# Kernel optimization log

Measured on AMD Instinct MI355X. Metric: run time of the kernel, lower is better.

The kernel has to match this reference:

```python
import jax, jax.numpy as jnp
import numpy as np

B, S, D, H, E, K = 4, 2048, 1024, 2048, 8, 2


def setup_inputs() -> dict:
    key = jax.random.key(0)
    ks = jax.random.split(key, 5)
    x = jax.random.normal(ks[0], (B, S, D), dtype=jnp.float32)
    Wr = jax.random.normal(ks[1], (D, E), dtype=jnp.float32) * 0.02  # router weight
    w1 = jax.random.normal(ks[2], (E, D, H), dtype=jnp.float32) * 0.02  # gate proj per expert
    w3 = jax.random.normal(ks[3], (E, D, H), dtype=jnp.float32) * 0.02  # up proj per expert
    w2 = jax.random.normal(ks[4], (E, H, D), dtype=jnp.float32) * 0.02  # down proj per expert
    return {"x": x, "Wr": Wr, "w1": w1, "w2": w2, "w3": w3}


def reference(x, Wr, w1, w2, w3):
    b, s, d = x.shape
    e = Wr.shape[1]
    flat = x.reshape(b * s, d)                      # [T, D]
    logits = flat @ Wr                              # [T, E]
    probs = jax.nn.softmax(logits, axis=-1)
    vals, idx = jax.lax.top_k(probs, K)             # [T, K]
    weights = vals / jnp.sum(vals, axis=-1, keepdims=True)
    onehot = jax.nn.one_hot(idx, e, dtype=flat.dtype)   # [T, K, E]
    cw = jnp.einsum('tke,tk->te', onehot, weights)      # combine weight per (token, expert)

    # naive dense: every expert computes every token, masked by combine weights
    out = jnp.zeros_like(flat)
    for ei in range(e):  # fixed small structural loop over experts
        h = jax.nn.silu(flat @ w1[ei]) * (flat @ w3[ei])   # [T, H]
        out = out + (h @ w2[ei]) * cw[:, ei:ei + 1]

    # aux load-balancing loss (usage uses any() over top-k slots, as in torch code)
    usage = (onehot.sum(axis=1) > 0).astype(flat.dtype).mean(axis=0)  # [E]
    prob_mass = probs.mean(axis=0)                                     # [E]
    aux_loss = e * jnp.sum(usage * prob_mass)
    return out.reshape(b, s, d), aux_loss
```

## Files before the change

kernel.cpp:

```cpp
#include <hip/hip_runtime.h>
#include <hip/hip_bf16.h>
#include <cstdint>
#include <cstddef>

#define T_TOK 8192
#define DIM   1024
#define HID   2048
#define NE    8
#define CAP   2816

#define SLOT  32768

typedef __attribute__((ext_vector_type(8))) short bf16x8;
typedef __attribute__((ext_vector_type(4))) float f32x4;
using bf16 = __hip_bfloat16;

__device__ __forceinline__ void gload16(const bf16* g, bf16* l) {
    __builtin_amdgcn_global_load_lds(
        (const __attribute__((address_space(1))) unsigned int*)(g),
        (__attribute__((address_space(3))) unsigned int*)(l), 16, 0, 0);
}
__device__ __forceinline__ float b2f(unsigned short u) {
    return __uint_as_float(((unsigned int)u) << 16);
}
#define MFMA16(a, b, c) __builtin_amdgcn_mfma_f32_16x16x32_bf16((a), (b), (c), 0, 0, 0)
#define BARRIER() asm volatile("s_barrier" ::: "memory")
#define WAITVM8() asm volatile("s_waitcnt vmcnt(8)" ::: "memory")
#define WAITVM0() asm volatile("s_waitcnt vmcnt(0)" ::: "memory")

__global__ __launch_bounds__(256) void k_transpose_all(const float* __restrict__ w1,
                                                       const float* __restrict__ w3,
                                                       const float* __restrict__ w2,
                                                       bf16* __restrict__ w1t,
                                                       bf16* __restrict__ w3t,
                                                       bf16* __restrict__ w2t) {
    __shared__ float tile[64][65];
    int z = blockIdx.z;
    const float* in = (z == 0) ? w1 : (z == 1) ? w3 : w2;
    bf16* out = (z == 0) ? w1t : (z == 1) ? w3t : w2t;
    int R = (z == 2) ? HID : DIM;
    int C = (z == 2) ? DIM : HID;
    int e = blockIdx.y;
    int ct = C >> 6;
    int r0 = (blockIdx.x / ct) << 6;
    int c0 = (blockIdx.x % ct) << 6;
    const float* src = in + (size_t)e * R * C;
    bf16* dst = out + (size_t)e * R * C;
    int s = threadIdx.x & 15, g = threadIdx.x >> 4;
#pragma unroll
    for (int j = 0; j < 4; ++j) {
        int row = j * 16 + g;
        float4 v = *(const float4*)(src + (size_t)(r0 + row) * C + c0 + s * 4);
        tile[row][s * 4 + 0] = v.x; tile[row][s * 4 + 1] = v.y;
        tile[row][s * 4 + 2] = v.z; tile[row][s * 4 + 3] = v.w;
    }
    __syncthreads();
#pragma unroll
    for (int j = 0; j < 4; ++j) {
        int c = j * 16 + g;
        int r = s * 4;
        bf16 o[4] = {__float2bfloat16(tile[r][c]),     __float2bfloat16(tile[r + 1][c]),
                     __float2bfloat16(tile[r + 2][c]), __float2bfloat16(tile[r + 3][c])};
        *(uint2*)(dst + (size_t)(c0 + c) * R + r0 + r) = *(const uint2*)o;
    }
}

__global__ __launch_bounds__(256) void k_logits(const float* __restrict__ x,
                                                const float* __restrict__ Wr,
                                                float* __restrict__ logits,
                                                bf16* __restrict__ xb) {
    __shared__ float wl[NE][DIM];
    for (int o = threadIdx.x; o < NE * DIM; o += 256) {
        int e = o >> 10, d = o & (DIM - 1);
        wl[e][d] = Wr[d * NE + e];
    }
    __syncthreads();
    int wid = threadIdx.x >> 6, lane = threadIdx.x & 63;
    int t = blockIdx.x * 4 + wid;
    const float* xr = x + (size_t)t * DIM;
    double acc[NE];
#pragma unroll
    for (int e = 0; e < NE; ++e) acc[e] = 0.0;
#pragma unroll
    for (int i = 0; i < DIM / 256; ++i) {
        int base = i * 256 + lane * 4;
        float4 v = *(const float4*)(xr + base);
        bf16 o[4] = {__float2bfloat16(v.x), __float2bfloat16(v.y),
                     __float2bfloat16(v.z), __float2bfloat16(v.w)};
        *(uint2*)(xb + (size_t)t * DIM + base) = *(const uint2*)o;
#pragma unroll
        for (int e = 0; e < NE; ++e)
            acc[e] += (double)v.x * wl[e][base] + (double)v.y * wl[e][base + 1]
                    + (double)v.z * wl[e][base + 2] + (double)v.w * wl[e][base + 3];
    }
#pragma unroll
    for (int e = 0; e < NE; ++e) {
        double v = acc[e];
        for (int m = 32; m >= 1; m >>= 1) v += __shfl_xor(v, m);
        if (lane == 0) logits[t * NE + e] = (float)v;
    }
}

__global__ __launch_bounds__(256) void k_route(const float* __restrict__ logits,
                                               int* counts, int* seg_tok, float* seg_w,
                                               int* slotpos, float* probsum) {
    int t = blockIdx.x * 256 + threadIdx.x;
    float l[NE];
#pragma unroll
    for (int e = 0; e < NE; ++e) l[e] = logits[t * NE + e];
    float mx = l[0];
#pragma unroll
    for (int e = 1; e < NE; ++e) mx = fmaxf(mx, l[e]);
    float p[NE], s = 0.f;
#pragma unroll
    for (int e = 0; e < NE; ++e) { p[e] = expf(l[e] - mx); s += p[e]; }
    float inv = 1.f / s;
#pragma unroll
    for (int e = 0; e < NE; ++e) p[e] *= inv;
    int e0 = 0; float v0 = p[0];
#pragma unroll
    for (int e = 1; e < NE; ++e) if (p[e] > v0) { v0 = p[e]; e0 = e; }
    int e1 = -1; float v1 = -1.f;
#pragma unroll
    for (int e = 0; e < NE; ++e) if (e != e0 && p[e] > v1) { v1 = p[e]; e1 = e; }
    float wsum = v0 + v1;
    float w0 = v0 / wsum, w1 = v1 / wsum;

    int lane = threadIdx.x & 63, wid = threadIdx.x >> 6;
    __shared__ float ps[4][NE];
#pragma unroll
    for (int e = 0; e < NE; ++e) {
        float v = p[e];
        for (int m = 32; m >= 1; m >>= 1) v += __shfl_xor(v, m);
        if (lane == 0) ps[wid][e] = v;
    }
    __syncthreads();
    if (threadIdx.x < NE) {
        float v = ps[0][threadIdx.x] + ps[1][threadIdx.x] + ps[2][threadIdx.x] + ps[3][threadIdx.x];
        atomicAdd(&probsum[threadIdx.x], v);
    }
    for (int slot = 0; slot < 2; ++slot) {
        int   e  = slot ? e1 : e0;
        float wv = slot ? w1 : w0;
#pragma unroll
        for (int ex = 0; ex < NE; ++ex) {
            unsigned long long m = __ballot(e == ex);
            if (e == ex) {
                int leader = __ffsll(m) - 1;
                int base = 0;
                if (lane == leader) base = atomicAdd(&counts[ex], __popcll(m));
                base = __shfl(base, leader);
                int pos = base + (int)__popcll(m & ((1ull << lane) - 1ull));
                if (pos < CAP) {
                    seg_tok[ex * CAP + pos] = t;
                    seg_w[ex * CAP + pos]  = wv;
                    slotpos[2 * t + slot]  = ex * CAP + pos;
                } else {
                    slotpos[2 * t + slot]  = -1;
                }
            }
        }
    }
}

__global__ __launch_bounds__(512, 2) void k_gemm1(const bf16* __restrict__ xb,
                                                  const bf16* __restrict__ w1t,
                                                  const bf16* __restrict__ w3t,
                                                  const int* __restrict__ counts,
                                                  const int* __restrict__ seg_tok,
                                                  bf16* __restrict__ h) {
    __shared__ __align__(16) bf16 lds[2 * SLOT];
    __shared__ int toks[256];
    const int NTL = HID / 128;
    int flat = blockIdx.y * gridDim.x + blockIdx.x;
    int cpx  = (gridDim.x * NE) >> 3;
    int swz  = (flat & 7) * cpx + (flat >> 3);
    int e    = swz / gridDim.x;
    int tile = swz % gridDim.x;
    int mtile = tile / NTL, ntile = tile % NTL;
    int cnt = counts[e]; if (cnt > CAP) cnt = CAP;
    if (mtile * 256 >= cnt) return;

    int tx = threadIdx.x, lane = tx & 63, wid = tx >> 6;
    for (int i = tx; i < 256; i += 512) {
        int slot = mtile * 256 + i;
        toks[i] = seg_tok[e * CAP + (slot < cnt ? slot : 0)];
    }
    __syncthreads();

    int l3 = lane >> 3, l7 = lane & 7, l15 = lane & 15, lh = lane >> 4;
    int swzco = (l7 ^ l3) << 3;
    const bf16* ap0 = xb + (size_t)toks[  0 + wid * 8 + l3] * DIM + swzco;
    const bf16* ap1 = xb + (size_t)toks[ 64 + wid * 8 + l3] * DIM + swzco;
    const bf16* ap2 = xb + (size_t)toks[128 + wid * 8 + l3] * DIM + swzco;
    const bf16* ap3 = xb + (size_t)toks[192 + wid * 8 + l3] * DIM + swzco;
    const bf16* bg0 = w1t + ((size_t)e * HID + ntile * 128 +  0 + wid * 8 + l3) * DIM + swzco;
    const bf16* bg1 = w1t + ((size_t)e * HID + ntile * 128 + 64 + wid * 8 + l3) * DIM + swzco;
    const bf16* bu0 = w3t + ((size_t)e * HID + ntile * 128 +  0 + wid * 8 + l3) * DIM + swzco;
    const bf16* bu1 = w3t + ((size_t)e * HID + ntile * 128 + 64 + wid * 8 + l3) * DIM + swzco;
    int wbase = wid * 512;
    int wm = wid >> 2, wn = wid & 3;

    f32x4 accg[8][2], accu[8][2];
    f32x4 zero4 = {0.f, 0.f, 0.f, 0.f};
#pragma unroll
    for (int m = 0; m < 8; ++m)
#pragma unroll
        for (int n = 0; n < 2; ++n) { accg[m][n] = zero4; accu[m][n] = zero4; }

#define G1_STAGE(ss, ko) do { \
        gload16(ap0 + (ko), lds + (ss) +     0 + wbase); \
        gload16(ap1 + (ko), lds + (ss) +  4096 + wbase); \
        gload16(ap2 + (ko), lds + (ss) +  8192 + wbase); \
        gload16(ap3 + (ko), lds + (ss) + 12288 + wbase); \
        gload16(bg0 + (ko), lds + (ss) + 16384 + wbase); \
        gload16(bg1 + (ko), lds + (ss) + 20480 + wbase); \
        gload16(bu0 + (ko), lds + (ss) + 24576 + wbase); \
        gload16(bu1 + (ko), lds + (ss) + 28672 + wbase); } while (0)

#define G1_PHASE(cs, mh, ks) do { \
        int cex = ((((ks) << 2) | lh) ^ l7) << 3; \
        const bf16* Ab = lds + (cs) + (wm * 128 + (mh) * 64 + l15) * 64 + cex; \
        bf16x8 a0 = *(const bf16x8*)(Ab); \
        bf16x8 a1 = *(const bf16x8*)(Ab + 1024); \
        bf16x8 a2 = *(const bf16x8*)(Ab + 2048); \
        bf16x8 a3 = *(const bf16x8*)(Ab + 3072); \
        const bf16* Bb = lds + (cs) + 16384 + (wn * 32 + l15) * 64 + cex; \
        bf16x8 g0 = *(const bf16x8*)(Bb); \
        bf16x8 g1 = *(const bf16x8*)(Bb + 1024); \
        bf16x8 u0 = *(const bf16x8*)(Bb + 8192); \
        bf16x8 u1 = *(const bf16x8*)(Bb + 9216); \
        __builtin_amdgcn_s_setprio(1); \
        accg[(mh)*4+0][0] = MFMA16(a0, g0, accg[(mh)*4+0][0]); \
        accg[(mh)*4+1][0] = MFMA16(a1, g0, accg[(mh)*4+1][0]); \
        accg[(mh)*4+2][0] = MFMA16(a2, g0, accg[(mh)*4+2][0]); \
        accg[(mh)*4+3][0] = MFMA16(a3, g0, accg[(mh)*4+3][0]); \
        accg[(mh)*4+0][1] = MFMA16(a0, g1, accg[(mh)*4+0][1]); \
        accg[(mh)*4+1][1] = MFMA16(a1, g1, accg[(mh)*4+1][1]); \
        accg[(mh)*4+2][1] = MFMA16(a2, g1, accg[(mh)*4+2][1]); \
        accg[(mh)*4+3][1] = MFMA16(a3, g1, accg[(mh)*4+3][1]); \
        accu[(mh)*4+0][0] = MFMA16(a0, u0, accu[(mh)*4+0][0]); \
        accu[(mh)*4+1][0] = MFMA16(a1, u0, accu[(mh)*4+1][0]); \
        accu[(mh)*4+2][0] = MFMA16(a2, u0, accu[(mh)*4+2][0]); \
        accu[(mh)*4+3][0] = MFMA16(a3, u0, accu[(mh)*4+3][0]); \
        accu[(mh)*4+0][1] = MFMA16(a0, u1, accu[(mh)*4+0][1]); \
        accu[(mh)*4+1][1] = MFMA16(a1, u1, accu[(mh)*4+1][1]); \
        accu[(mh)*4+2][1] = MFMA16(a2, u1, accu[(mh)*4+2][1]); \
        accu[(mh)*4+3][1] = MFMA16(a3, u1, accu[(mh)*4+3][1]); \
        __builtin_amdgcn_s_setprio(0); } while (0)

    G1_STAGE(0, 0);
    const int NT = DIM / 64;
    int cs = 0, ns = SLOT;
#pragma unroll 1
    for (int T = 0; T < NT; ++T) {
        if (T + 1 < NT) { G1_STAGE(ns, (T + 1) * 64); WAITVM8(); }
        else WAITVM0();
        BARRIER();
        G1_PHASE(cs, 0, 0); G1_PHASE(cs, 0, 1);
        G1_PHASE(cs, 1, 0); G1_PHASE(cs, 1, 1);
        BARRIER();
        int tmp = cs; cs = ns; ns = tmp;
    }

    bf16* hdst = h + ((size_t)e * CAP + (size_t)mtile * 256) * HID + ntile * 128;
#pragma unroll
    for (int m = 0; m < 8; ++m)
#pragma unroll
        for (int n = 0; n < 2; ++n)
#pragma unroll
            for (int r = 0; r < 4; ++r) {
                int row = wm * 128 + m * 16 + lh * 4 + r;
                int col = wn * 32 + n * 16 + l15;
                float gg = accg[m][n][r], uu = accu[m][n][r];
                float hv = gg / (1.f + __expf(-gg)) * uu;
                hdst[(size_t)row * HID + col] = __float2bfloat16(hv);
            }
#undef G1_STAGE
#undef G1_PHASE
}

__global__ __launch_bounds__(512, 2) void k_gemm2(const bf16* __restrict__ h,
                                                  const bf16* __restrict__ w2t,
                                                  const int* __restrict__ counts,
                                                  const float* __restrict__ seg_w,
                                                  bf16* __restrict__ ybuf) {
    __shared__ __align__(16) bf16 lds[2 * SLOT];
    __shared__ float wts[256];
    const int NTL = DIM / 256;
    int flat = blockIdx.y * gridDim.x + blockIdx.x;
    int cpx  = (gridDim.x * NE) >> 3;
    int swz  = (flat & 7) * cpx + (flat >> 3);
    int e    = swz / gridDim.x;
    int tile = swz % gridDim.x;
    int mtile = tile / NTL, ntile = tile % NTL;
    int cnt = counts[e]; if (cnt > CAP) cnt = CAP;
    if (mtile * 256 >= cnt) return;

    int tx = threadIdx.x, lane = tx & 63, wid = tx >> 6;
    for (int i = tx; i < 256; i += 512) {
        int slot = mtile * 256 + i;
        wts[i] = (slot < cnt) ? seg_w[e * CAP + slot] : 0.f;
    }
    __syncthreads();

    int l3 = lane >> 3, l7 = lane & 7, l15 = lane & 15, lh = lane >> 4;
    int swzco = (l7 ^ l3) << 3;
    const bf16* ap0 = h + ((size_t)e * CAP + mtile * 256 +   0 + wid * 8 + l3) * HID + swzco;
    const bf16* ap1 = h + ((size_t)e * CAP + mtile * 256 +  64 + wid * 8 + l3) * HID + swzco;
    const bf16* ap2 = h + ((size_t)e * CAP + mtile * 256 + 128 + wid * 8 + l3) * HID + swzco;
    const bf16* ap3 = h + ((size_t)e * CAP + mtile * 256 + 192 + wid * 8 + l3) * HID + swzco;
    const bf16* bp0 = w2t + ((size_t)e * DIM + ntile * 256 +   0 + wid * 8 + l3) * HID + swzco;
    const bf16* bp1 = w2t + ((size_t)e * DIM + ntile * 256 +  64 + wid * 8 + l3) * HID + swzco;
    const bf16* bp2 = w2t + ((size_t)e * DIM + ntile * 256 + 128 + wid * 8 + l3) * HID + swzco;
    const bf16* bp3 = w2t + ((size_t)e * DIM + ntile * 256 + 192 + wid * 8 + l3) * HID + swzco;
    int wbase = wid * 512;
    int wm = wid >> 2, wn = wid & 3;

    f32x4 acc[8][4];
    f32x4 zero4 = {0.f, 0.f, 0.f, 0.f};
#pragma unroll
    for (int m = 0; m < 8; ++m)
#pragma unroll
        for (int n = 0; n < 4; ++n) acc[m][n] = zero4;

#define G2_STAGE(ss, ko) do { \
        gload16(ap0 + (ko), lds + (ss) +     0 + wbase); \
        gload16(ap1 + (ko), lds + (ss) +  4096 + wbase); \
        gload16(ap2 + (ko), lds + (ss) +  8192 + wbase); \
        gload16(ap3 + (ko), lds + (ss) + 12288 + wbase); \
        gload16(bp0 + (ko), lds + (ss) + 16384 + wbase); \
        gload16(bp1 + (ko), lds + (ss) + 20480 + wbase); \
        gload16(bp2 + (ko), lds + (ss) + 24576 + wbase); \
        gload16(bp3 + (ko), lds + (ss) + 28672 + wbase); } while (0)

#define G2_PHASE(cs, mh, ks) do { \
        int cex = ((((ks) << 2) | lh) ^ l7) << 3; \
        const bf16* Ab = lds + (cs) + (wm * 128 + (mh) * 64 + l15) * 64 + cex; \
        bf16x8 a0 = *(const bf16x8*)(Ab); \
        bf16x8 a1 = *(const bf16x8*)(Ab + 1024); \
        bf16x8 a2 = *(const bf16x8*)(Ab + 2048); \
        bf16x8 a3 = *(const bf16x8*)(Ab + 3072); \
        const bf16* Bb = lds + (cs) + 16384 + (wn * 64 + l15) * 64 + cex; \
        bf16x8 b0 = *(const bf16x8*)(Bb); \
        bf16x8 b1 = *(const bf16x8*)(Bb + 1024); \
        bf16x8 b2 = *(const bf16x8*)(Bb + 2048); \
        bf16x8 b3 = *(const bf16x8*)(Bb + 3072); \
        __builtin_amdgcn_s_setprio(1); \
        acc[(mh)*4+0][0] = MFMA16(a0, b0, acc[(mh)*4+0][0]); \
        acc[(mh)*4+1][0] = MFMA16(a1, b0, acc[(mh)*4+1][0]); \
        acc[(mh)*4+2][0] = MFMA16(a2, b0, acc[(mh)*4+2][0]); \
        acc[(mh)*4+3][0] = MFMA16(a3, b0, acc[(mh)*4+3][0]); \
        acc[(mh)*4+0][1] = MFMA16(a0, b1, acc[(mh)*4+0][1]); \
        acc[(mh)*4+1][1] = MFMA16(a1, b1, acc[(mh)*4+1][1]); \
        acc[(mh)*4+2][1] = MFMA16(a2, b1, acc[(mh)*4+2][1]); \
        acc[(mh)*4+3][1] = MFMA16(a3, b1, acc[(mh)*4+3][1]); \
        acc[(mh)*4+0][2] = MFMA16(a0, b2, acc[(mh)*4+0][2]); \
        acc[(mh)*4+1][2] = MFMA16(a1, b2, acc[(mh)*4+1][2]); \
        acc[(mh)*4+2][2] = MFMA16(a2, b2, acc[(mh)*4+2][2]); \
        acc[(mh)*4+3][2] = MFMA16(a3, b2, acc[(mh)*4+3][2]); \
        acc[(mh)*4+0][3] = MFMA16(a0, b3, acc[(mh)*4+0][3]); \
        acc[(mh)*4+1][3] = MFMA16(a1, b3, acc[(mh)*4+1][3]); \
        acc[(mh)*4+2][3] = MFMA16(a2, b3, acc[(mh)*4+2][3]); \
        acc[(mh)*4+3][3] = MFMA16(a3, b3, acc[(mh)*4+3][3]); \
        __builtin_amdgcn_s_setprio(0); } while (0)

    G2_STAGE(0, 0);
    const int NT = HID / 64;
    int cs = 0, ns = SLOT;
#pragma unroll 1
    for (int T = 0; T < NT; ++T) {
        if (T + 1 < NT) { G2_STAGE(ns, (T + 1) * 64); WAITVM8(); }
        else WAITVM0();
        BARRIER();
        G2_PHASE(cs, 0, 0); G2_PHASE(cs, 0, 1);
        G2_PHASE(cs, 1, 0); G2_PHASE(cs, 1, 1);
        BARRIER();
        int tmp = cs; cs = ns; ns = tmp;
    }

    bf16* ydst = ybuf + ((size_t)e * CAP + (size_t)mtile * 256) * DIM + ntile * 256;
#pragma unroll
    for (int m = 0; m < 8; ++m)
#pragma unroll
        for (int n = 0; n < 4; ++n)
#pragma unroll
            for (int r = 0; r < 4; ++r) {
                int row = wm * 128 + m * 16 + lh * 4 + r;
                int col = wn * 64 + n * 16 + l15;
                ydst[(size_t)row * DIM + col] = __float2bfloat16(acc[m][n][r] * wts[row]);
            }
#undef G2_STAGE
#undef G2_PHASE
}

__global__ __launch_bounds__(256) void k_combine(const bf16* __restrict__ yb,
                                                 const int* __restrict__ slotpos,
                                                 float* __restrict__ out) {
    int t = blockIdx.x;
    int s0 = slotpos[2 * t], s1 = slotpos[2 * t + 1];
    int d = threadIdx.x * 4;
    float4 a = {0.f, 0.f, 0.f, 0.f};
    if (s0 >= 0) {
        ushort4 v = *(const ushort4*)(yb + (size_t)s0 * DIM + d);
        a.x += b2f(v.x); a.y += b2f(v.y); a.z += b2f(v.z); a.w += b2f(v.w);
    }
    if (s1 >= 0) {
        ushort4 v = *(const ushort4*)(yb + (size_t)s1 * DIM + d);
        a.x += b2f(v.x); a.y += b2f(v.y); a.z += b2f(v.z); a.w += b2f(v.w);
    }
    *(float4*)(out + (size_t)t * DIM + d) = a;
}

__global__ void k_aux(const int* __restrict__ counts, const float* __restrict__ probsum,
                      float* __restrict__ outaux) {
    if (threadIdx.x == 0 && blockIdx.x == 0) {
        float s = 0.f;
        for (int e = 0; e < NE; ++e)
            s += ((float)counts[e] / (float)T_TOK) * (probsum[e] / (float)T_TOK);
        *outaux = (float)NE * s;
    }
}

extern "C" void kernel_launch(void* const* d_in, const int* in_sizes, int n_in,
                              void* d_out, int out_size, void* d_ws, size_t ws_size,
                              hipStream_t stream) {
    const float* x  = (const float*)d_in[0];
    const float* Wr = (const float*)d_in[1];
    const float* w1 = (const float*)d_in[2];
    const float* w2 = (const float*)d_in[3];
    const float* w3 = (const float*)d_in[4];
    float* out = (float*)d_out;

    char* ws = (char*)d_ws;
    size_t off = 0;
    auto alloc = [&](size_t bytes) { void* p = ws + off; off += (bytes + 255) & ~(size_t)255; return p; };
    bf16*  xb      = (bf16*)alloc((size_t)T_TOK * DIM * 2);
    bf16*  w1t     = (bf16*)alloc((size_t)NE * HID * DIM * 2);
    bf16*  w3t     = (bf16*)alloc((size_t)NE * HID * DIM * 2);
    bf16*  w2t     = (bf16*)alloc((size_t)NE * DIM * HID * 2);
    bf16*  hbuf    = (bf16*)alloc((size_t)NE * CAP * HID * 2);
    float* logits  = (float*)alloc((size_t)T_TOK * NE * 4);
    int*   counts  = (int*)alloc(256);
    int*   segtok  = (int*)alloc((size_t)NE * CAP * 4);
    float* segw    = (float*)alloc((size_t)NE * CAP * 4);
    int*   slotpos = (int*)alloc((size_t)T_TOK * 2 * 4);
    float* probsum = (float*)alloc(256);
    bf16*  ybuf    = w1t;
    (void)ws_size; (void)in_sizes; (void)n_in;

    hipMemsetAsync(counts, 0, 256, stream);
    hipMemsetAsync(probsum, 0, 256, stream);

    k_logits<<<T_TOK / 4, 256, 0, stream>>>(x, Wr, logits, xb);
    k_route<<<T_TOK / 256, 256, 0, stream>>>(logits, counts, segtok, segw, slotpos, probsum);

    dim3 gt((DIM / 64) * (HID / 64), NE, 3);
    k_transpose_all<<<gt, 256, 0, stream>>>(w1, w3, w2, w1t, w3t, w2t);

    dim3 g1((CAP / 256) * (HID / 128), NE);
    k_gemm1<<<g1, 512, 0, stream>>>(xb, w1t, w3t, counts, segtok, hbuf);
    dim3 g2((CAP / 256) * (DIM / 256), NE);
    k_gemm2<<<g2, 512, 0, stream>>>(hbuf, w2t, counts, segw, ybuf);

    k_combine<<<T_TOK, 256, 0, stream>>>(ybuf, slotpos, out);
    k_aux<<<1, 64, 0, stream>>>(counts, probsum, out + (size_t)T_TOK * DIM);
}
```

Measured before the change: 459.4 us.

## Switch GEMM mainloops to 4-stage BK=32 pipeline with split A/B staging

Both expert GEMM kernels move from a double-buffered K=64 tile to a four-slot ring of K=32 tiles with prefetch distance two. A and B loads are issued separately: A for step k+2 before the first barrier, B after the first half of the MFMAs. The LDS layout and XOR swizzle change to match 32-wide rows. The aim is to hide global-load latency better and keep loads in flight across barriers. The cost is two barriers per smaller K step, a more intricate vmcnt wait schedule, and a risk of bank conflicts with the new swizzle.

New measurement: 471.9 us. 2.7% more time.

```diff
diff --git a/kernel.cpp b/kernel.cpp
--- a/kernel.cpp
+++ b/kernel.cpp
@@ -9,8 +9,6 @@
 #define NE    8
 #define CAP   2816
 
-#define SLOT  32768
-
 typedef __attribute__((ext_vector_type(8))) short bf16x8;
 typedef __attribute__((ext_vector_type(4))) float f32x4;
 using bf16 = __hip_bfloat16;
@@ -25,7 +23,8 @@
 }
 #define MFMA16(a, b, c) __builtin_amdgcn_mfma_f32_16x16x32_bf16((a), (b), (c), 0, 0, 0)
 #define BARRIER() asm volatile("s_barrier" ::: "memory")
-#define WAITVM8() asm volatile("s_waitcnt vmcnt(8)" ::: "memory")
+#define WAITVM6() asm volatile("s_waitcnt vmcnt(6)" ::: "memory")
+#define WAITVM4() asm volatile("s_waitcnt vmcnt(4)" ::: "memory")
 #define WAITVM0() asm volatile("s_waitcnt vmcnt(0)" ::: "memory")
 
 __global__ __launch_bounds__(256) void k_transpose_all(const float* __restrict__ w1,
@@ -169,7 +168,7 @@
                                                   const int* __restrict__ counts,
                                                   const int* __restrict__ seg_tok,
                                                   bf16* __restrict__ h) {
-    __shared__ __align__(16) bf16 lds[2 * SLOT];
+    __shared__ __align__(16) bf16 lds[65536];
     __shared__ int toks[256];
     const int NTL = HID / 128;
     int flat = blockIdx.y * gridDim.x + blockIdx.x;
@@ -188,18 +187,20 @@
     }
     __syncthreads();
 
-    int l3 = lane >> 3, l7 = lane & 7, l15 = lane & 15, lh = lane >> 4;
-    int swzco = (l7 ^ l3) << 3;
-    const bf16* ap0 = xb + (size_t)toks[  0 + wid * 8 + l3] * DIM + swzco;
-    const bf16* ap1 = xb + (size_t)toks[ 64 + wid * 8 + l3] * DIM + swzco;
-    const bf16* ap2 = xb + (size_t)toks[128 + wid * 8 + l3] * DIM + swzco;
-    const bf16* ap3 = xb + (size_t)toks[192 + wid * 8 + l3] * DIM + swzco;
-    const bf16* bg0 = w1t + ((size_t)e * HID + ntile * 128 +  0 + wid * 8 + l3) * DIM + swzco;
-    const bf16* bg1 = w1t + ((size_t)e * HID + ntile * 128 + 64 + wid * 8 + l3) * DIM + swzco;
-    const bf16* bu0 = w3t + ((size_t)e * HID + ntile * 128 +  0 + wid * 8 + l3) * DIM + swzco;
-    const bf16* bu1 = w3t + ((size_t)e * HID + ntile * 128 + 64 + wid * 8 + l3) * DIM + swzco;
-    int wbase = wid * 512;
+    int sr  = tx >> 2;
+    int sc8 = (((tx & 3) ^ ((tx >> 3) & 3)) << 3);
+    const bf16* sApLo = xb + (size_t)toks[sr]       * DIM + sc8;
+    const bf16* sApHi = xb + (size_t)toks[128 + sr] * DIM + sc8;
+    const bf16* sBg   = w1t + ((size_t)e * HID + ntile * 128 + sr) * DIM + sc8;
+    const bf16* sBu   = w3t + ((size_t)e * HID + ntile * 128 + sr) * DIM + sc8;
+    bf16* dA = lds + tx * 8;
+    bf16* dB = lds + 32768 + tx * 8;
+
+    int l15 = lane & 15, lh = lane >> 4;
     int wm = wid >> 2, wn = wid & 3;
+    int ach = ((lh ^ ((l15 >> 1) & 3)) << 3);
+    const bf16* rA = lds + (wm * 128 + l15) * 32 + ach;
+    const bf16* rB = lds + 32768 + (wn * 32 + l15) * 32 + ach;
 
     f32x4 accg[8][2], accu[8][2];
     f32x4 zero4 = {0.f, 0.f, 0.f, 0.f};
@@ -208,60 +209,70 @@
 #pragma unroll
         for (int n = 0; n < 2; ++n) { accg[m][n] = zero4; accu[m][n] = zero4; }
 
-#define G1_STAGE(ss, ko) do { \
-        gload16(ap0 + (ko), lds + (ss) +     0 + wbase); \
-        gload16(ap1 + (ko), lds + (ss) +  4096 + wbase); \
-        gload16(ap2 + (ko), lds + (ss) +  8192 + wbase); \
-        gload16(ap3 + (ko), lds + (ss) + 12288 + wbase); \
-        gload16(bg0 + (ko), lds + (ss) + 16384 + wbase); \
-        gload16(bg1 + (ko), lds + (ss) + 20480 + wbase); \
-        gload16(bu0 + (ko), lds + (ss) + 24576 + wbase); \
-        gload16(bu1 + (ko), lds + (ss) + 28672 + wbase); } while (0)
-
-#define G1_PHASE(cs, mh, ks) do { \
-        int cex = ((((ks) << 2) | lh) ^ l7) << 3; \
-        const bf16* Ab = lds + (cs) + (wm * 128 + (mh) * 64 + l15) * 64 + cex; \
-        bf16x8 a0 = *(const bf16x8*)(Ab); \
-        bf16x8 a1 = *(const bf16x8*)(Ab + 1024); \
-        bf16x8 a2 = *(const bf16x8*)(Ab + 2048); \
-        bf16x8 a3 = *(const bf16x8*)(Ab + 3072); \
-        const bf16* Bb = lds + (cs) + 16384 + (wn * 32 + l15) * 64 + cex; \
-        bf16x8 g0 = *(const bf16x8*)(Bb); \
-        bf16x8 g1 = *(const bf16x8*)(Bb + 1024); \
-        bf16x8 u0 = *(const bf16x8*)(Bb + 8192); \
-        bf16x8 u1 = *(const bf16x8*)(Bb + 9216); \
-        __builtin_amdgcn_s_setprio(1); \
-        accg[(mh)*4+0][0] = MFMA16(a0, g0, accg[(mh)*4+0][0]); \
-        accg[(mh)*4+1][0] = MFMA16(a1, g0, accg[(mh)*4+1][0]); \
-        accg[(mh)*4+2][0] = MFMA16(a2, g0, accg[(mh)*4+2][0]); \
-        accg[(mh)*4+3][0] = MFMA16(a3, g0, accg[(mh)*4+3][0]); \
-        accg[(mh)*4+0][1] = MFMA16(a0, g1, accg[(mh)*4+0][1]); \
-        accg[(mh)*4+1][1] = MFMA16(a1, g1, accg[(mh)*4+1][1]); \
-        accg[(mh)*4+2][1] = MFMA16(a2, g1, accg[(mh)*4+2][1]); \
-        accg[(mh)*4+3][1] = MFMA16(a3, g1, accg[(mh)*4+3][1]); \
-        accu[(mh)*4+0][0] = MFMA16(a0, u0, accu[(mh)*4+0][0]); \
-        accu[(mh)*4+1][0] = MFMA16(a1, u0, accu[(mh)*4+1][0]); \
-        accu[(mh)*4+2][0] = MFMA16(a2, u0, accu[(mh)*4+2][0]); \
-        accu[(mh)*4+3][0] = MFMA16(a3, u0, accu[(mh)*4+3][0]); \
-        accu[(mh)*4+0][1] = MFMA16(a0, u1, accu[(mh)*4+0][1]); \
-        accu[(mh)*4+1][1] = MFMA16(a1, u1, accu[(mh)*4+1][1]); \
-        accu[(mh)*4+2][1] = MFMA16(a2, u1, accu[(mh)*4+2][1]); \
-        accu[(mh)*4+3][1] = MFMA16(a3, u1, accu[(mh)*4+3][1]); \
-        __builtin_amdgcn_s_setprio(0); } while (0)
-
-    G1_STAGE(0, 0);
-    const int NT = DIM / 64;
-    int cs = 0, ns = SLOT;
+#define STAGE_A1(s, ko) do { \
+        gload16(sApLo + (ko), dA + (s) * 8192); \
+        gload16(sApHi + (ko), dA + (s) * 8192 + 4096); } while (0)
+#define STAGE_B1(s, ko) do { \
+        gload16(sBg + (ko), dB + (s) * 8192); \
+        gload16(sBu + (ko), dB + (s) * 8192 + 4096); } while (0)
+
+    STAGE_A1(0, 0);  STAGE_B1(0, 0);
+    STAGE_A1(1, 32); STAGE_B1(1, 32);
+
+    const int NT = DIM / 32;
+    bf16x8 g0, g1, u0, u1;
 #pragma unroll 1
-    for (int T = 0; T < NT; ++T) {
-        if (T + 1 < NT) { G1_STAGE(ns, (T + 1) * 64); WAITVM8(); }
-        else WAITVM0();
+    for (int k = 0; k < NT; ++k) {
+        int cs = (k & 3) * 8192, ps = (k + 2) & 3;
+        bool st = (k + 2 < NT);
+        int ko = (k + 2) * 32;
+        if (st) STAGE_A1(ps, ko);
+        if (k < NT - 2) WAITVM6(); else if (k < NT - 1) WAITVM4(); else WAITVM0();
         BARRIER();
-        G1_PHASE(cs, 0, 0); G1_PHASE(cs, 0, 1);
-        G1_PHASE(cs, 1, 0); G1_PHASE(cs, 1, 1);
+        {
+            const bf16* Ab = rA + cs;
+            bf16x8 a0 = *(const bf16x8*)(Ab);
+            bf16x8 a1 = *(const bf16x8*)(Ab + 512);
+            bf16x8 a2 = *(const bf16x8*)(Ab + 1024);
+            bf16x8 a3 = *(const bf16x8*)(Ab + 1536);
+            const bf16* Bb = rB + cs;
+            g0 = *(const bf16x8*)(Bb);
+            g1 = *(const bf16x8*)(Bb + 512);
+            u0 = *(const bf16x8*)(Bb + 4096);
+            u1 = *(const bf16x8*)(Bb + 4608);
+            __builtin_amdgcn_s_setprio(1);
+            accg[0][0] = MFMA16(a0, g0, accg[0][0]); accg[1][0] = MFMA16(a1, g0, accg[1][0]);
+            accg[2][0] = MFMA16(a2, g0, accg[2][0]); accg[3][0] = MFMA16(a3, g0, accg[3][0]);
+            accg[0][1] = MFMA16(a0, g1, accg[0][1]); accg[1][1] = MFMA16(a1, g1, accg[1][1]);
+            accg[2][1] = MFMA16(a2, g1, accg[2][1]); accg[3][1] = MFMA16(a3, g1, accg[3][1]);
+            accu[0][0] = MFMA16(a0, u0, accu[0][0]); accu[1][0] = MFMA16(a1, u0, accu[1][0]);
+            accu[2][0] = MFMA16(a2, u0, accu[2][0]); accu[3][0] = MFMA16(a3, u0, accu[3][0]);
+            accu[0][1] = MFMA16(a0, u1, accu[0][1]); accu[1][1] = MFMA16(a1, u1, accu[1][1]);
+            accu[2][1] = MFMA16(a2, u1, accu[2][1]); accu[3][1] = MFMA16(a3, u1, accu[3][1]);
+            __builtin_amdgcn_s_setprio(0);
+        }
+        if (st) STAGE_B1(ps, ko);
         BARRIER();
-        int tmp = cs; cs = ns; ns = tmp;
-    }
+        {
+            const bf16* Ab = rA + cs + 2048;
+            bf16x8 a4 = *(const bf16x8*)(Ab);
+            bf16x8 a5 = *(const bf16x8*)(Ab + 512);
+            bf16x8 a6 = *(const bf16x8*)(Ab + 1024);
+            bf16x8 a7 = *(const bf16x8*)(Ab + 1536);
+            __builtin_amdgcn_s_setprio(1);
+            accg[4][0] = MFMA16(a4, g0, accg[4][0]); accg[5][0] = MFMA16(a5, g0, accg[5][0]);
+            accg[6][0] = MFMA16(a6, g0, accg[6][0]); accg[7][0] = MFMA16(a7, g0, accg[7][0]);
+            accg[4][1] = MFMA16(a4, g1, accg[4][1]); accg[5][1] = MFMA16(a5, g1, accg[5][1]);
+            accg[6][1] = MFMA16(a6, g1, accg[6][1]); accg[7][1] = MFMA16(a7, g1, accg[7][1]);
+            accu[4][0] = MFMA16(a4, u0, accu[4][0]); accu[5][0] = MFMA16(a5, u0, accu[5][0]);
+            accu[6][0] = MFMA16(a6, u0, accu[6][0]); accu[7][0] = MFMA16(a7, u0, accu[7][0]);
+            accu[4][1] = MFMA16(a4, u1, accu[4][1]); accu[5][1] = MFMA16(a5, u1, accu[5][1]);
+            accu[6][1] = MFMA16(a6, u1, accu[6][1]); accu[7][1] = MFMA16(a7, u1, accu[7][1]);
+            __builtin_amdgcn_s_setprio(0);
+        }
+    }
+#undef STAGE_A1
+#undef STAGE_B1
 
     bf16* hdst = h + ((size_t)e * CAP + (size_t)mtile * 256) * HID + ntile * 128;
 #pragma unroll
@@ -276,8 +287,6 @@
                 float hv = gg / (1.f + __expf(-gg)) * uu;
                 hdst[(size_t)row * HID + col] = __float2bfloat16(hv);
             }
-#undef G1_STAGE
-#undef G1_PHASE
 }
 
 __global__ __launch_bounds__(512, 2) void k_gemm2(const bf16* __restrict__ h,
@@ -285,7 +294,7 @@
                                                   const int* __restrict__ counts,
                                                   const float* __restrict__ seg_w,
                                                   bf16* __restrict__ ybuf) {
-    __shared__ __align__(16) bf16 lds[2 * SLOT];
+    __shared__ __align__(16) bf16 lds[65536];
     __shared__ float wts[256];
     const int NTL = DIM / 256;
     int flat = blockIdx.y * gridDim.x + blockIdx.x;
@@ -304,18 +313,20 @@
     }
     __syncthreads();
 
-    int l3 = lane >> 3, l7 = lane & 7, l15 = lane & 15, lh = lane >> 4;
-    int swzco = (l7 ^ l3) << 3;
-    const bf16* ap0 = h + ((size_t)e * CAP + mtile * 256 +   0 + wid * 8 + l3) * HID + swzco;
-    const bf16* ap1 = h + ((size_t)e * CAP + mtile * 256 +  64 + wid * 8 + l3) * HID + swzco;
-    const bf16* ap2 = h + ((size_t)e * CAP + mtile * 256 + 128 + wid * 8 + l3) * HID + swzco;
-    const bf16* ap3 = h + ((size_t)e * CAP + mtile * 256 + 192 + wid * 8 + l3) * HID + swzco;
-    const bf16* bp0 = w2t + ((size_t)e * DIM + ntile * 256 +   0 + wid * 8 + l3) * HID + swzco;
-    const bf16* bp1 = w2t + ((size_t)e * DIM + ntile * 256 +  64 + wid * 8 + l3) * HID + swzco;
-    const bf16* bp2 = w2t + ((size_t)e * DIM + ntile * 256 + 128 + wid * 8 + l3) * HID + swzco;
-    const bf16* bp3 = w2t + ((size_t)e * DIM + ntile * 256 + 192 + wid * 8 + l3) * HID + swzco;
-    int wbase = wid * 512;
+    int sr  = tx >> 2;
+    int sc8 = (((tx & 3) ^ ((tx >> 3) & 3)) << 3);
+    const bf16* sApLo = h + ((size_t)e * CAP + mtile * 256 + sr) * HID + sc8;
+    const bf16* sApHi = h + ((size_t)e * CAP + mtile * 256 + 128 + sr) * HID + sc8;
+    const bf16* sBpLo = w2t + ((size_t)e * DIM + ntile * 256 + sr) * HID + sc8;
+    const bf16* sBpHi = w2t + ((size_t)e * DIM + ntile * 256 + 128 + sr) * HID + sc8;
+    bf16* dA = lds + tx * 8;
+    bf16* dB = lds + 32768 + tx * 8;
+
+    int l15 = lane & 15, lh = lane >> 4;
     int wm = wid >> 2, wn = wid & 3;
+    int ach = ((lh ^ ((l15 >> 1) & 3)) << 3);
+    const bf16* rA = lds + (wm * 128 + l15) * 32 + ach;
+    const bf16* rB = lds + 32768 + (wn * 64 + l15) * 32 + ach;
 
     f32x4 acc[8][4];
     f32x4 zero4 = {0.f, 0.f, 0.f, 0.f};
@@ -324,60 +335,70 @@
 #pragma unroll
         for (int n = 0; n < 4; ++n) acc[m][n] = zero4;
 
-#define G2_STAGE(ss, ko) do { \
-        gload16(ap0 + (ko), lds + (ss) +     0 + wbase); \
-        gload16(ap1 + (ko), lds + (ss) +  4096 + wbase); \
-        gload16(ap2 + (ko), lds + (ss) +  8192 + wbase); \
-        gload16(ap3 + (ko), lds + (ss) + 12288 + wbase); \
-        gload16(bp0 + (ko), lds + (ss) + 16384 + wbase); \
-        gload16(bp1 + (ko), lds + (ss) + 20480 + wbase); \
-        gload16(bp2 + (ko), lds + (ss) + 24576 + wbase); \
-        gload16(bp3 + (ko), lds + (ss) + 28672 + wbase); } while (0)
-
-#define G2_PHASE(cs, mh, ks) do { \
-        int cex = ((((ks) << 2) | lh) ^ l7) << 3; \
-        const bf16* Ab = lds + (cs) + (wm * 128 + (mh) * 64 + l15) * 64 + cex; \
-        bf16x8 a0 = *(const bf16x8*)(Ab); \
-        bf16x8 a1 = *(const bf16x8*)(Ab + 1024); \
-        bf16x8 a2 = *(const bf16x8*)(Ab + 2048); \
-        bf16x8 a3 = *(const bf16x8*)(Ab + 3072); \
-        const bf16* Bb = lds + (cs) + 16384 + (wn * 64 + l15) * 64 + cex; \
-        bf16x8 b0 = *(const bf16x8*)(Bb); \
-        bf16x8 b1 = *(const bf16x8*)(Bb + 1024); \
-        bf16x8 b2 = *(const bf16x8*)(Bb + 2048); \
-        bf16x8 b3 = *(const bf16x8*)(Bb + 3072); \
-        __builtin_amdgcn_s_setprio(1); \
-        acc[(mh)*4+0][0] = MFMA16(a0, b0, acc[(mh)*4+0][0]); \
-        acc[(mh)*4+1][0] = MFMA16(a1, b0, acc[(mh)*4+1][0]); \
-        acc[(mh)*4+2][0] = MFMA16(a2, b0, acc[(mh)*4+2][0]); \
-        acc[(mh)*4+3][0] = MFMA16(a3, b0, acc[(mh)*4+3][0]); \
-        acc[(mh)*4+0][1] = MFMA16(a0, b1, acc[(mh)*4+0][1]); \
-        acc[(mh)*4+1][1] = MFMA16(a1, b1, acc[(mh)*4+1][1]); \
-        acc[(mh)*4+2][1] = MFMA16(a2, b1, acc[(mh)*4+2][1]); \
-        acc[(mh)*4+3][1] = MFMA16(a3, b1, acc[(mh)*4+3][1]); \
-        acc[(mh)*4+0][2] = MFMA16(a0, b2, acc[(mh)*4+0][2]); \
-        acc[(mh)*4+1][2] = MFMA16(a1, b2, acc[(mh)*4+1][2]); \
-        acc[(mh)*4+2][2] = MFMA16(a2, b2, acc[(mh)*4+2][2]); \
-        acc[(mh)*4+3][2] = MFMA16(a3, b2, acc[(mh)*4+3][2]); \
-        acc[(mh)*4+0][3] = MFMA16(a0, b3, acc[(mh)*4+0][3]); \
-        acc[(mh)*4+1][3] = MFMA16(a1, b3, acc[(mh)*4+1][3]); \
-        acc[(mh)*4+2][3] = MFMA16(a2, b3, acc[(mh)*4+2][3]); \
-        acc[(mh)*4+3][3] = MFMA16(a3, b3, acc[(mh)*4+3][3]); \
-        __builtin_amdgcn_s_setprio(0); } while (0)
-
-    G2_STAGE(0, 0);
-    const int NT = HID / 64;
-    int cs = 0, ns = SLOT;
+#define STAGE_A2(s, ko) do { \
+        gload16(sApLo + (ko), dA + (s) * 8192); \
+        gload16(sApHi + (ko), dA + (s) * 8192 + 4096); } while (0)
+#define STAGE_B2(s, ko) do { \
+        gload16(sBpLo + (ko), dB + (s) * 8192); \
+        gload16(sBpHi + (ko), dB + (s) * 8192 + 4096); } while (0)
+
+    STAGE_A2(0, 0);  STAGE_B2(0, 0);
+    STAGE_A2(1, 32); STAGE_B2(1, 32);
+
+    const int NT = HID / 32;
+    bf16x8 b0, b1, b2, b3;
 #pragma unroll 1
-    for (int T = 0; T < NT; ++T) {
-        if (T + 1 < NT) { G2_STAGE(ns, (T + 1) * 64); WAITVM8(); }
-        else WAITVM0();
+    for (int k = 0; k < NT; ++k) {
+        int cs = (k & 3) * 8192, ps = (k + 2) & 3;
+        bool st = (k + 2 < NT);
+        int ko = (k + 2) * 32;
+        if (st) STAGE_A2(ps, ko);
+        if (k < NT - 2) WAITVM6(); else if (k < NT - 1) WAITVM4(); else WAITVM0();
         BARRIER();
-        G2_PHASE(cs, 0, 0); G2_PHASE(cs, 0, 1);
-        G2_PHASE(cs, 1, 0); G2_PHASE(cs, 1, 1);
+        {
+            const bf16* Ab = rA + cs;
+            bf16x8 a0 = *(const bf16x8*)(Ab);
+            bf16x8 a1 = *(const bf16x8*)(Ab + 512);
+            bf16x8 a2 = *(const bf16x8*)(Ab + 1024);
+            bf16x8 a3 = *(const bf16x8*)(Ab + 1536);
+            const bf16* Bb = rB + cs;
+            b0 = *(const bf16x8*)(Bb);
+            b1 = *(const bf16x8*)(Bb + 512);
+            b2 = *(const bf16x8*)(Bb + 1024);
+            b3 = *(const bf16x8*)(Bb + 1536);
+            __builtin_amdgcn_s_setprio(1);
+            acc[0][0] = MFMA16(a0, b0, acc[0][0]); acc[1][0] = MFMA16(a1, b0, acc[1][0]);
+            acc[2][0] = MFMA16(a2, b0, acc[2][0]); acc[3][0] = MFMA16(a3, b0, acc[3][0]);
+            acc[0][1] = MFMA16(a0, b1, acc[0][1]); acc[1][1] = MFMA16(a1, b1, acc[1][1]);
+            acc[2][1] = MFMA16(a2, b1, acc[2][1]); acc[3][1] = MFMA16(a3, b1, acc[3][1]);
+            acc[0][2] = MFMA16(a0, b2, acc[0][2]); acc[1][2] = MFMA16(a1, b2, acc[1][2]);
+            acc[2][2] = MFMA16(a2, b2, acc[2][2]); acc[3][2] = MFMA16(a3, b2, acc[3][2]);
+            acc[0][3] = MFMA16(a0, b3, acc[0][3]); acc[1][3] = MFMA16(a1, b3, acc[1][3]);
+            acc[2][3] = MFMA16(a2, b3, acc[2][3]); acc[3][3] = MFMA16(a3, b3, acc[3][3]);
+            __builtin_amdgcn_s_setprio(0);
+        }
+        if (st) STAGE_B2(ps, ko);
         BARRIER();
-        int tmp = cs; cs = ns; ns = tmp;
-    }
+        {
+            const bf16* Ab = rA + cs + 2048;
+            bf16x8 a4 = *(const bf16x8*)(Ab);
+            bf16x8 a5 = *(const bf16x8*)(Ab + 512);
+            bf16x8 a6 = *(const bf16x8*)(Ab + 1024);
+            bf16x8 a7 = *(const bf16x8*)(Ab + 1536);
+            __builtin_amdgcn_s_setprio(1);
+            acc[4][0] = MFMA16(a4, b0, acc[4][0]); acc[5][0] = MFMA16(a5, b0, acc[5][0]);
+            acc[6][0] = MFMA16(a6, b0, acc[6][0]); acc[7][0] = MFMA16(a7, b0, acc[7][0]);
+            acc[4][1] = MFMA16(a4, b1, acc[4][1]); acc[5][1] = MFMA16(a5, b1, acc[5][1]);
+            acc[6][1] = MFMA16(a6, b1, acc[6][1]); acc[7][1] = MFMA16(a7, b1, acc[7][1]);
+            acc[4][2] = MFMA16(a4, b2, acc[4][2]); acc[5][2] = MFMA16(a5, b2, acc[5][2]);
+            acc[6][2] = MFMA16(a6, b2, acc[6][2]); acc[7][2] = MFMA16(a7, b2, acc[7][2]);
+            acc[4][3] = MFMA16(a4, b3, acc[4][3]); acc[5][3] = MFMA16(a5, b3, acc[5][3]);
+            acc[6][3] = MFMA16(a6, b3, acc[6][3]); acc[7][3] = MFMA16(a7, b3, acc[7][3]);
+            __builtin_amdgcn_s_setprio(0);
+        }
+    }
+#undef STAGE_A2
+#undef STAGE_B2
 
     bf16* ydst = ybuf + ((size_t)e * CAP + (size_t)mtile * 256) * DIM + ntile * 256;
 #pragma unroll
@@ -390,8 +411,6 @@
                 int col = wn * 64 + n * 16 + l15;
                 ydst[(size_t)row * DIM + col] = __float2bfloat16(acc[m][n][r] * wts[row]);
             }
-#undef G2_STAGE
-#undef G2_PHASE
 }
 
 __global__ __launch_bounds__(256) void k_combine(const bf16* __restrict__ yb,
```
